# Kernel optimization log

Measured on AMD Instinct MI355X. Metric: run time of the kernel, lower is better.

## Reference

```python
import jax, jax.numpy as jnp
import numpy as np

B, S, D = 8, 8192, 64
N_HASHES = 8
BUCKET_SIZE = 64
N_BUCKETS = S // BUCKET_SIZE  # 128
SELF_ATTN_VALUE = -5e4  # torch reformer TOKEN_SELF_ATTN_VALUE


def setup_inputs() -> dict:
    key = jax.random.key(0)
    k1, k2, k3 = jax.random.split(key, 3)
    qk = jax.random.normal(k1, (B, S, D), dtype=jnp.float32)
    v = jax.random.normal(k2, (B, S, D), dtype=jnp.float32)
    # LSH random rotations: (dim, n_hashes, n_buckets // 2), shared across batch/heads
    rotations = jax.random.normal(k3, (D, N_HASHES, N_BUCKETS // 2), dtype=jnp.float32)
    return {"qk": qk, "v": v, "rotations": rotations, "query_len": S}


def _look_one_back(x):
    # concatenate each chunk with the preceding chunk (wrapping) along the kv axis
    x_extra = jnp.concatenate([x[:, -1:], x[:, :-1]], axis=1)
    return jnp.concatenate([x, x_extra], axis=2)


def _lsh_bucketed_dots(qk, v, rotations):
    batch, seqlen, dim = qk.shape
    n_buckets = seqlen // BUCKET_SIZE
    # --- hash vectors: rotate, concat with negation, argmax -> bucket ids ---
    rotated = jnp.einsum('btf,fhi->bhti', qk, rotations)           # (B, H, S, nb/2)
    rotated = jnp.concatenate([rotated, -rotated], axis=-1)        # (B, H, S, nb)
    buckets = jnp.argmax(rotated, axis=-1)                         # (B, H, S) int
    offsets = (jnp.arange(N_HASHES) * n_buckets)[None, :, None]    # disjoint per round
    buckets = (buckets + offsets).reshape(batch, -1)               # (B, H*S)

    # --- stable bucket sort via composite key (all keys unique) ---
    ticker = jnp.arange(N_HASHES * seqlen)[None, :]                # (1, H*S)
    buckets_and_t = seqlen * buckets + (ticker % seqlen)
    sticker = jnp.argsort(buckets_and_t, axis=-1)                  # sort permutation
    undo_sort = jnp.argsort(sticker, axis=-1)                      # inverse permutation
    st = sticker % seqlen                                          # original token ids

    # --- gather tokens into bucket order ---
    sqk = jnp.take_along_axis(qk, st[..., None], axis=1)           # (B, H*S, D)
    sv = jnp.take_along_axis(v, st[..., None], axis=1)

    n_chunks = N_HASHES * n_buckets
    bq_t = st.reshape(batch, n_chunks, BUCKET_SIZE)                # (B, C, bs)
    bqk = sqk.reshape(batch, n_chunks, BUCKET_SIZE, dim)
    bv = sv.reshape(batch, n_chunks, BUCKET_SIZE, dim)

    bq = bqk
    bk = bqk / (jnp.linalg.norm(bqk, axis=-1, keepdims=True) + 1e-6)  # unit-length keys

    bk = _look_one_back(bk)       # (B, C, 2*bs, D)
    bv = _look_one_back(bv)
    bkv_t = _look_one_back(bq_t)  # (B, C, 2*bs)

    dots = jnp.einsum('buie,buje->buij', bq, bk) * (dim ** -0.5)   # (B, C, bs, 2*bs)
    self_mask = bq_t[:, :, :, None] == bkv_t[:, :, None, :]
    dots = jnp.where(self_mask, SELF_ATTN_VALUE, dots)
    return dots, undo_sort, bv


def reference(qk, v, rotations, query_len):
    batch, seqlen, dim = qk.shape
    dots, undo_sort, bv = _lsh_bucketed_dots(qk, v, rotations)
    dots_logsumexp = jax.nn.logsumexp(dots, axis=-1, keepdims=True)
    p = jnp.exp(dots - dots_logsumexp)                             # per-bucket softmax
    bo = jnp.einsum('buij,buje->buie', p, bv)                      # (B, C, bs, D)
    so = bo.reshape(batch, -1, dim)                                # (B, H*S, D)
    slogits = dots_logsumexp.reshape(batch, -1)                    # (B, H*S)
    # undo the bucket sort
    o = jnp.take_along_axis(so, undo_sort[..., None], axis=1)
    logits = jnp.take_along_axis(slogits, undo_sort, axis=1)
    o = o.reshape(batch, N_HASHES, seqlen, dim)[:, :, :query_len]
    logits = logits.reshape(batch, N_HASHES, seqlen, 1)[:, :, :query_len]
    # combine across hash rounds, weighted by per-round logsumexp
    probs = jnp.exp(logits - jax.nn.logsumexp(logits, axis=1, keepdims=True))
    out = jnp.sum(o * probs, axis=1)                               # (B, query_len, D)
    return out
```

## Files before the change

kernel.cpp:

```cpp
#include <hip/hip_runtime.h>
#include <math.h>

#define B_  8
#define S_  8192
#define D_  64
#define H_  8
#define NB_ 128
#define NC_ 1024
#define REP_CAP 65536
#define T2_ 2e-3f

typedef _Float16 f16x8 __attribute__((ext_vector_type(8)));
typedef _Float16 f16x2 __attribute__((ext_vector_type(2)));
typedef float    f32x4 __attribute__((ext_vector_type(4)));
typedef unsigned int uint_;

#define MFMA16(A, Bv, C) __builtin_amdgcn_mfma_f32_16x16x32_f16(A, Bv, C, 0, 0, 0)

__global__ __launch_bounds__(256) void prep_rot_kernel(
    const float* __restrict__ rot, _Float16* __restrict__ rotHi,
    _Float16* __restrict__ rotLo, int* __restrict__ cnt)
{
  __shared__ float rs[64 * 64];
  const int tid = threadIdx.x, h = blockIdx.x;
  if (h == 0 && tid == 0) *cnt = 0;
#pragma unroll
  for (int it = 0; it < 16; ++it) {
    const int f = it * 4 + (tid >> 6), i = tid & 63;
    rs[f * 64 + i] = rot[f * 512 + h * 64 + i];
  }
  __syncthreads();
  const int i = tid & 63, grp = tid >> 6;
  _Float16 hi[16], lo[16];
#pragma unroll
  for (int ff = 0; ff < 16; ++ff) {
    const float x = rs[(grp * 16 + ff) * 64 + i];
    hi[ff] = (_Float16)x;
    lo[ff] = (_Float16)(x - (float)hi[ff]);
  }
  f16x8* dH = (f16x8*)(rotHi + h * 4096 + i * 64 + grp * 16);
  f16x8* dL = (f16x8*)(rotLo + h * 4096 + i * 64 + grp * 16);
  dH[0] = ((f16x8*)hi)[0]; dH[1] = ((f16x8*)hi)[1];
  dL[0] = ((f16x8*)lo)[0]; dL[1] = ((f16x8*)lo)[1];
}

__global__ __launch_bounds__(256) void prep_tok_kernel(
    const float* __restrict__ qk, const float* __restrict__ v,
    _Float16* __restrict__ q16, _Float16* __restrict__ kn16,
    _Float16* __restrict__ v16)
{
  const int gt = blockIdx.x * 64 + (threadIdx.x >> 2);
  const int qu = threadIdx.x & 3;
  const size_t off = (size_t)gt * 64 + qu * 16;
  float x[16];
#pragma unroll
  for (int k = 0; k < 4; ++k) ((float4*)x)[k] = ((const float4*)(qk + off))[k];
  float ss = 0.f;
#pragma unroll
  for (int k = 0; k < 16; ++k) ss = fmaf(x[k], x[k], ss);
  ss += __shfl_xor(ss, 1); ss += __shfl_xor(ss, 2);
  const float inv = 0.125f / (sqrtf(ss) + 1e-6f);
  f16x8 qh[2], kn[2];
#pragma unroll
  for (int j = 0; j < 16; ++j) {
    qh[j >> 3][j & 7] = (_Float16)x[j];
    kn[j >> 3][j & 7] = (_Float16)(x[j] * inv);
  }
  ((f16x8*)(q16  + off))[0] = qh[0]; ((f16x8*)(q16  + off))[1] = qh[1];
  ((f16x8*)(kn16 + off))[0] = kn[0]; ((f16x8*)(kn16 + off))[1] = kn[1];
  float y[16];
#pragma unroll
  for (int k = 0; k < 4; ++k) ((float4*)y)[k] = ((const float4*)(v + off))[k];
  f16x8 vv[2];
#pragma unroll
  for (int j = 0; j < 16; ++j) vv[j >> 3][j & 7] = (_Float16)y[j];
  ((f16x8*)(v16 + off))[0] = vv[0]; ((f16x8*)(v16 + off))[1] = vv[1];
}

__global__ __launch_bounds__(256) void hash_kernel(
    const float* __restrict__ qk,
    const _Float16* __restrict__ rotHi, const _Float16* __restrict__ rotLo,
    int* __restrict__ bucket, int* __restrict__ cnt, int2* __restrict__ list)
{
  __shared__ _Float16 rH[64 * 72];
  __shared__ _Float16 rL[64 * 72];
  const int tid  = threadIdx.x;
  const int tile = blockIdx.x & 127;
  const int b    = blockIdx.x >> 7;
  const int lane = tid & 63, w = tid >> 6;
  const int m16  = lane & 15, qd = lane >> 4;

  const int t = tile * 64 + w * 16 + m16;
  f16x8 BH0, BH1, BL0, BL1;
  {
    const float* src = qk + ((size_t)b * S_ + t) * 64 + 8 * qd;
    float x[16];
    ((float4*)x)[0] = ((const float4*)src)[0];
    ((float4*)x)[1] = ((const float4*)(src + 4))[0];
    ((float4*)x)[2] = ((const float4*)(src + 32))[0];
    ((float4*)x)[3] = ((const float4*)(src + 36))[0];
#pragma unroll
    for (int j = 0; j < 8; ++j) {
      const _Float16 h0 = (_Float16)x[j];
      BH0[j] = h0; BL0[j] = (_Float16)(x[j] - (float)h0);
      const _Float16 h1 = (_Float16)x[j + 8];
      BH1[j] = h1; BL1[j] = (_Float16)(x[j + 8] - (float)h1);
    }
  }
  const int srow = tid >> 2, scol = (tid & 3) * 16;
  const uint_ qd16 = (uint_)(qd << 4);

#pragma unroll 1
  for (int h = 0; h < 8; ++h) {
    __syncthreads();
    {
      const _Float16* sH = rotHi + h * 4096 + srow * 64 + scol;
      const _Float16* sL = rotLo + h * 4096 + srow * 64 + scol;
      *(f16x8*)(rH + srow * 72 + scol)     = ((const f16x8*)sH)[0];
      *(f16x8*)(rH + srow * 72 + scol + 8) = ((const f16x8*)sH)[1];
      *(f16x8*)(rL + srow * 72 + scol)     = ((const f16x8*)sL)[0];
      *(f16x8*)(rL + srow * 72 + scol + 8) = ((const f16x8*)sL)[1];
    }
    __syncthreads();

    f32x4 acc[4];
#pragma unroll
    for (int mt = 0; mt < 4; ++mt) acc[mt] = (f32x4){0.f, 0.f, 0.f, 0.f};
#pragma unroll
    for (int mt = 0; mt < 4; ++mt) {
      const _Float16* aH = rH + (16 * mt + m16) * 72 + 8 * qd;
      const _Float16* aL = rL + (16 * mt + m16) * 72 + 8 * qd;
      const f16x8 AH0 = *(const f16x8*)aH;
      const f16x8 AH1 = *(const f16x8*)(aH + 32);
      const f16x8 AL0 = *(const f16x8*)aL;
      const f16x8 AL1 = *(const f16x8*)(aL + 32);
      acc[mt] = MFMA16(AH0, BH0, acc[mt]);
      acc[mt] = MFMA16(AH1, BH1, acc[mt]);
      acc[mt] = MFMA16(AH0, BL0, acc[mt]);
      acc[mt] = MFMA16(AH1, BL1, acc[mt]);
      acc[mt] = MFMA16(AL0, BH0, acc[mt]);
      acc[mt] = MFMA16(AL1, BH1, acc[mt]);
    }

    float v1M = -1e30f, v2M = -1e30f, v1m = 1e30f, v2m = 1e30f;
#pragma unroll
    for (int mt = 0; mt < 4; ++mt)
#pragma unroll
      for (int rg = 0; rg < 4; ++rg) {
        uint_ u = __float_as_uint(acc[mt][rg]);
        u = (u & 0xFFFFFFC0u) | qd16 | (uint_)((mt << 2) | rg);
        const float xk = __uint_as_float(u);
        v2M = __builtin_amdgcn_fmed3f(v1M, v2M, xk);
        v1M = fmaxf(v1M, xk);
        v2m = __builtin_amdgcn_fmed3f(v1m, v2m, xk);
        v1m = fminf(v1m, xk);
      }
#pragma unroll
    for (int off = 16; off <= 32; off <<= 1) {
      const float o1M = __shfl_xor(v1M, off), o2M = __shfl_xor(v2M, off);
      v2M = __builtin_amdgcn_fmed3f(v1M, o1M, fmaxf(v2M, o2M));
      v1M = fmaxf(v1M, o1M);
      const float o1m = __shfl_xor(v1m, off), o2m = __shfl_xor(v2m, off);
      v2m = __builtin_amdgcn_fmed3f(v1m, o1m, fminf(v2m, o2m));
      v1m = fminf(v1m, o1m);
    }
    if (qd == 0) {
      const uint_ cM = __float_as_uint(v1M) & 63u;
      const uint_ cm = __float_as_uint(v1m) & 63u;
      const int ixM = 16 * (int)((cM >> 2) & 3u) + 4 * (int)(cM >> 4) + (int)(cM & 3u);
      const int ixm = 16 * (int)((cm >> 2) & 3u) + 4 * (int)(cm >> 4) + (int)(cm & 3u);
      const int bkt = (v1M >= -v1m) ? ixM : 64 + ixm;
      bucket[((size_t)(b * 8 + h)) * S_ + t] = bkt;
      const bool flag = ((v1M - v2M) < T2_) | ((v2m - v1m) < T2_) |
                        (fabsf(v1M + v1m) < T2_);
      if (flag) {
        const int s = atomicAdd(cnt, 1);
        if (s < REP_CAP) list[s] = make_int2(b * 8 + h, t);
      }
    }
  }
}

__global__ __launch_bounds__(256) void repair_kernel(
    const float* __restrict__ qk, const float* __restrict__ rot,
    const int* __restrict__ cnt, const int2* __restrict__ list,
    int* __restrict__ bucket)
{
  const int n = min(*cnt, REP_CAP);
  const int lane = threadIdx.x & 63;
  const int wid  = (blockIdx.x * 256 + threadIdx.x) >> 6;
  const int nw   = gridDim.x * 4;
  for (int idx = wid; idx < n; idx += nw) {
    const int bh = list[idx].x, t = list[idx].y;
    const int b = bh >> 3, hh = bh & 7;
    const float* qrow = qk + ((size_t)b * S_ + t) * D_;
    const float* rcol = rot + hh * 64 + lane;
    double acc = 0.0;
#pragma unroll 8
    for (int f = 0; f < 64; ++f)
      acc = fma((double)qrow[f], (double)rcol[(size_t)f * 512], acc);
    double vM = acc; int iM = lane;
    double vm = acc; int im = lane;
#pragma unroll
    for (int off = 32; off >= 1; off >>= 1) {
      const double voM = __shfl_xor(vM, off); const int ioM = __shfl_xor(iM, off);
      if (voM > vM || (voM == vM && ioM < iM)) { vM = voM; iM = ioM; }
      const double vom = __shfl_xor(vm, off); const int iom = __shfl_xor(im, off);
      if (vom < vm || (vom == vm && iom < im)) { vm = vom; im = iom; }
    }
    if (lane == 0) {
      const int bkt = (vM >= -vm) ? iM : 64 + im;
      bucket[(size_t)bh * S_ + t] = bkt;
    }
  }
}

__global__ __launch_bounds__(1024) void sort_kernel(
    const int* __restrict__ bucket, int* __restrict__ st)
{
  __shared__ uint_ hist[64 * 128];
  __shared__ unsigned short lb[S_];
  __shared__ int off[128];
  const int tid = threadIdx.x;
  const int bh  = blockIdx.x;
  const size_t base = (size_t)bh * S_;

#pragma unroll
  for (int k = 0; k < 8; ++k) hist[tid + k * 1024] = 0;
  __syncthreads();

#pragma unroll
  for (int k = 0; k < 8; ++k) {
    const int t = k * 1024 + tid;
    const int bk = bucket[base + t];
    lb[t] = (unsigned short)bk;
    const int g = t >> 6;
    atomicAdd(&hist[(g & 63) * 128 + bk], 1u << (16 * (g >> 6)));
  }
  __syncthreads();

  if (tid < 128) {
    uint_ s = 0;
#pragma unroll
    for (int g = 0; g < 64; ++g) {
      const uint_ wv = hist[g * 128 + tid];
      s += (wv & 0xFFFFu) + (wv >> 16);
    }
    off[tid] = (int)s;
  }
  __syncthreads();
  if (tid == 0) {
    int run = 0;
    for (int k = 0; k < 128; ++k) { const int c = off[k]; off[k] = run; run += c; }
  }
  __syncthreads();
  if (tid < 128) {
    uint_ run = (uint_)off[tid];
#pragma unroll
    for (int g = 0; g < 64; ++g) {
      const uint_ wv = hist[g * 128 + tid];
      hist[g * 128 + tid] = (wv & 0xFFFF0000u) | run;
      run += (wv & 0xFFFFu);
    }
#pragma unroll
    for (int g = 0; g < 64; ++g) {
      const uint_ wv = hist[g * 128 + tid];
      hist[g * 128 + tid] = (wv & 0xFFFFu) | (run << 16);
      run += (wv >> 16);
    }
  }
  __syncthreads();

  const int lane = tid & 63, wv_ = tid >> 6;
  const int b = bh >> 3, h = bh & 7;
  const size_t stb = (size_t)b * (H_ * S_) + (size_t)h * S_;
  const unsigned long long ltmask = (1ull << lane) - 1ull;
#pragma unroll
  for (int k = 0; k < 8; ++k) {
    const int g = wv_ * 8 + k;
    const int t = g * 64 + lane;
    const int bk = (int)lb[t];
    unsigned long long same = ~0ull;
#pragma unroll
    for (int bit = 0; bit < 7; ++bit) {
      const unsigned long long m = __ballot((bk >> bit) & 1);
      same &= ((bk >> bit) & 1) ? m : ~m;
    }
    const int rloc = __popcll(same & ltmask);
    const uint_ wd = hist[(g & 63) * 128 + bk];
    const int gbase = (int)((wd >> (16 * (g >> 6))) & 0xFFFFu);
    st[stb + gbase + rloc] = t;
  }
}

__global__ __launch_bounds__(256, 4) void attn_kernel(
    const _Float16* __restrict__ q16, const _Float16* __restrict__ kn16,
    const _Float16* __restrict__ v16, const int* __restrict__ st,
    _Float16* __restrict__ so, float* __restrict__ slog)
{
  __shared__ _Float16 sQ[64 * 72];
  __shared__ _Float16 sK[64 * 72];
  __shared__ _Float16 sP[64 * 136];
  __shared__ int sIds[128];

  const int tid = threadIdx.x;
  const int c   = blockIdx.x & (NC_ - 1);
  const int b   = blockIdx.x >> 10;
  const int cm1 = (c + NC_ - 1) & (NC_ - 1);
  const size_t bst = (size_t)b * (H_ * S_);
  const size_t row0 = bst + (size_t)c * 64;
  const size_t row1 = bst + (size_t)cm1 * 64;

  const int lane = tid & 63;
  const int w    = tid >> 6;
  const int m16  = lane & 15;
  const int qd   = lane >> 4;

  if (tid < 128) sIds[tid] = (tid < 64) ? st[row0 + tid] : st[row1 + tid - 64];

  const int r = tid >> 2, qu = tid & 3;
  {
    const int tok = st[row0 + r];
    const size_t go = ((size_t)b * S_ + tok) * 64 + qu * 16;
    const f16x8* sq = (const f16x8*)(q16 + go);
    *(f16x8*)(sQ + r * 72 + qu * 16)     = sq[0];
    *(f16x8*)(sQ + r * 72 + qu * 16 + 8) = sq[1];
    const f16x8* sk = (const f16x8*)(kn16 + go);
    *(f16x8*)(sK + r * 72 + qu * 16)     = sk[0];
    *(f16x8*)(sK + r * 72 + qu * 16 + 8) = sk[1];
  }
  __syncthreads();

  f32x4 acc[8];
#pragma unroll
  for (int jt = 0; jt < 8; ++jt) acc[jt] = (f32x4){0.f, 0.f, 0.f, 0.f};

  const _Float16* qrow = sQ + (16 * w + m16) * 72;
  const f16x8 a0 = *(const f16x8*)(qrow + 8 * qd);
  const f16x8 a1 = *(const f16x8*)(qrow + 32 + 8 * qd);

#pragma unroll
  for (int jt = 0; jt < 4; ++jt) {
    const _Float16* krow = sK + (16 * jt + m16) * 72;
    const f16x8 b0 = *(const f16x8*)(krow + 8 * qd);
    const f16x8 b1 = *(const f16x8*)(krow + 32 + 8 * qd);
    acc[jt] = MFMA16(a0, b0, acc[jt]);
    acc[jt] = MFMA16(a1, b1, acc[jt]);
  }
  __syncthreads();

  {
    const int tok = st[row1 + r];
    const f16x8* sk = (const f16x8*)(kn16 + ((size_t)b * S_ + tok) * 64 + qu * 16);
    *(f16x8*)(sK + r * 72 + qu * 16)     = sk[0];
    *(f16x8*)(sK + r * 72 + qu * 16 + 8) = sk[1];
  }
  __syncthreads();

#pragma unroll
  for (int jt = 4; jt < 8; ++jt) {
    const _Float16* krow = sK + (16 * (jt - 4) + m16) * 72;
    const f16x8 b0 = *(const f16x8*)(krow + 8 * qd);
    const f16x8 b1 = *(const f16x8*)(krow + 32 + 8 * qd);
    acc[jt] = MFMA16(a0, b0, acc[jt]);
    acc[jt] = MFMA16(a1, b1, acc[jt]);
  }

  const int jp = tid >> 2;
  const int tok0 = sIds[2 * jp], tok1 = sIds[2 * jp + 1];
  f16x8 va[2], vb[2];
  {
    const f16x8* s0 = (const f16x8*)(v16 + ((size_t)b * S_ + tok0) * 64 + qu * 16);
    const f16x8* s1 = (const f16x8*)(v16 + ((size_t)b * S_ + tok1) * 64 + qu * 16);
    va[0] = s0[0]; va[1] = s0[1];
    vb[0] = s1[0]; vb[1] = s1[1];
  }

  int rid[4];
#pragma unroll
  for (int rg = 0; rg < 4; ++rg) rid[rg] = sIds[16 * w + 4 * qd + rg];
  float rmax[4] = {-1e30f, -1e30f, -1e30f, -1e30f};
#pragma unroll
  for (int jt = 0; jt < 8; ++jt) {
    const int cid = sIds[16 * jt + m16];
#pragma unroll
    for (int rg = 0; rg < 4; ++rg) {
      float x = acc[jt][rg];
      if (rid[rg] == cid) x = -5e4f;
      acc[jt][rg] = x;
      rmax[rg] = fmaxf(rmax[rg], x);
    }
  }
#pragma unroll
  for (int rg = 0; rg < 4; ++rg) {
    rmax[rg] = fmaxf(rmax[rg], __shfl_xor(rmax[rg], 1));
    rmax[rg] = fmaxf(rmax[rg], __shfl_xor(rmax[rg], 2));
    rmax[rg] = fmaxf(rmax[rg], __shfl_xor(rmax[rg], 4));
    rmax[rg] = fmaxf(rmax[rg], __shfl_xor(rmax[rg], 8));
  }
  float rsum[4] = {0.f, 0.f, 0.f, 0.f};
#pragma unroll
  for (int jt = 0; jt < 8; ++jt)
#pragma unroll
    for (int rg = 0; rg < 4; ++rg) {
      const float e = __expf(acc[jt][rg] - rmax[rg]);
      acc[jt][rg] = e;
      rsum[rg] += e;
    }
#pragma unroll
  for (int rg = 0; rg < 4; ++rg) {
    rsum[rg] += __shfl_xor(rsum[rg], 1);
    rsum[rg] += __shfl_xor(rsum[rg], 2);
    rsum[rg] += __shfl_xor(rsum[rg], 4);
    rsum[rg] += __shfl_xor(rsum[rg], 8);
  }
  float rinv[4];
#pragma unroll
  for (int rg = 0; rg < 4; ++rg) rinv[rg] = 1.f / rsum[rg];

  const int hh = c >> 7;
  const size_t hb = ((size_t)(b * 8 + hh)) * S_;
  if (m16 == 0) {
#pragma unroll
    for (int rg = 0; rg < 4; ++rg)
      slog[hb + rid[rg]] = rmax[rg] + __logf(rsum[rg]);
  }

#pragma unroll
  for (int jt = 0; jt < 8; ++jt)
#pragma unroll
    for (int rg = 0; rg < 4; ++rg)
      sP[(16 * w + 4 * qd + rg) * 136 + 16 * jt + m16] = (_Float16)acc[jt][rg];

  __syncthreads();

  {
    const int j = 2 * jp;
    _Float16* dst = (j < 64) ? (sK + j) : (sQ + (j - 64));
#pragma unroll
    for (int jj = 0; jj < 16; ++jj) {
      const int d = qu * 16 + jj;
      f16x2 pk; pk[0] = va[jj >> 3][jj & 7]; pk[1] = vb[jj >> 3][jj & 7];
      *(f16x2*)(dst + d * 72) = pk;
    }
  }
  __syncthreads();

  f32x4 oacc[4];
#pragma unroll
  for (int dt = 0; dt < 4; ++dt) oacc[dt] = (f32x4){0.f, 0.f, 0.f, 0.f};
  const _Float16* prow = sP + (16 * w + m16) * 136;
#pragma unroll
  for (int s = 0; s < 4; ++s) {
    const f16x8 ap = *(const f16x8*)(prow + 32 * s + 8 * qd);
    const _Float16* vbase = (s < 2) ? sK : sQ;
    const int col0 = 32 * (s & 1) + 8 * qd;
#pragma unroll
    for (int dt = 0; dt < 4; ++dt) {
      const f16x8 bv = *(const f16x8*)(vbase + (16 * dt + m16) * 72 + col0);
      oacc[dt] = MFMA16(ap, bv, oacc[dt]);
    }
  }

#pragma unroll
  for (int dt = 0; dt < 4; ++dt)
#pragma unroll
    for (int rg = 0; rg < 4; ++rg)
      so[(hb + rid[rg]) * 64 + 16 * dt + m16] = (_Float16)(oacc[dt][rg] * rinv[rg]);
}

__global__ __launch_bounds__(256) void combine_kernel(
    const _Float16* __restrict__ so, const float* __restrict__ slog,
    float* __restrict__ out)
{
  const int gt = blockIdx.x * 4 + (threadIdx.x >> 6);
  const int d  = threadIdx.x & 63;
  const int b  = gt >> 13;
  const int t  = gt & (S_ - 1);

  float l[8];
#pragma unroll
  for (int h = 0; h < 8; ++h)
    l[h] = slog[((size_t)(b * 8 + h)) * S_ + t];
  float m = l[0];
#pragma unroll
  for (int h = 1; h < 8; ++h) m = fmaxf(m, l[h]);
  float wv[8], W = 0.f;
#pragma unroll
  for (int h = 0; h < 8; ++h) { wv[h] = expf(l[h] - m); W += wv[h]; }
  const float iW = 1.f / W;
  float acc = 0.f;
#pragma unroll
  for (int h = 0; h < 8; ++h)
    acc = fmaf(wv[h], (float)so[(((size_t)(b * 8 + h)) * S_ + t) * 64 + d], acc);
  out[(size_t)gt * 64 + d] = acc * iW;
}

extern "C" void kernel_launch(void* const* d_in, const int* in_sizes, int n_in,
                              void* d_out, int out_size, void* d_ws, size_t ws_size,
                              hipStream_t stream)
{
  const float* qk  = (const float*)d_in[0];
  const float* v   = (const float*)d_in[1];
  const float* rot = (const float*)d_in[2];
  float* out = (float*)d_out;

  char* ws = (char*)d_ws;
  const size_t MB = 1ull << 20, KB = 1024;
  int*      bucket = (int*)      (ws + 0 * MB);
  int*      st     = (int*)      (ws + 2 * MB);
  float*    slog   = (float*)    (ws + 4 * MB);
  _Float16* q16    = (_Float16*) (ws + 8 * MB);
  _Float16* kn16   = (_Float16*) (ws + 16 * MB);
  _Float16* v16    = (_Float16*) (ws + 24 * MB);
  _Float16* rotHi  = (_Float16*) (ws + 32 * MB);
  _Float16* rotLo  = (_Float16*) (ws + 32 * MB + 64 * KB);
  int*      cnt    = (int*)      (ws + 32 * MB + 128 * KB);
  int2*     list   = (int2*)     (ws + 32 * MB + 192 * KB);
  _Float16* so     = (_Float16*) (ws + 33 * MB);
  if (ws_size < 98 * MB) return;

  hipLaunchKernelGGL(prep_rot_kernel, dim3(8),           dim3(256),  0, stream, rot, rotHi, rotLo, cnt);
  hipLaunchKernelGGL(prep_tok_kernel, dim3(1024),        dim3(256),  0, stream, qk, v, q16, kn16, v16);
  hipLaunchKernelGGL(hash_kernel,     dim3(8 * 128),     dim3(256),  0, stream, qk, rotHi, rotLo, bucket, cnt, list);
  hipLaunchKernelGGL(repair_kernel,   dim3(128),         dim3(256),  0, stream, qk, rot, cnt, list, bucket);
  hipLaunchKernelGGL(sort_kernel,     dim3(64),          dim3(1024), 0, stream, bucket, st);
  hipLaunchKernelGGL(attn_kernel,     dim3(B_ * NC_),    dim3(256),  0, stream, q16, kn16, v16, st, so, slog);
  hipLaunchKernelGGL(combine_kernel,  dim3(B_ * S_ / 4), dim3(256),  0, stream, so, slog, out);
}
```

Measured before the change: 209.2 us.

## Fuse token fp16 prep into hash kernel, read rotations directly, stage attn output

Merges prep_tok_kernel into hash_kernel so qk is read once and q16/kn16/v16 are written from the same loads, removing a launch and a full pass over qk. The rotation tiles are no longer staged through LDS with barriers; each wave loads rotation fragments straight from global/L2. The attention output is now staged through shared memory so the global scatter into so writes contiguous 32-byte rows per thread. Direct global rotation loads add L2 traffic per block, and the fused kernel carries more registers.

```diff
diff --git a/kernel.cpp b/kernel.cpp
--- a/kernel.cpp
+++ b/kernel.cpp
@@ -44,46 +44,13 @@
   dL[0] = ((f16x8*)lo)[0]; dL[1] = ((f16x8*)lo)[1];
 }
 
-__global__ __launch_bounds__(256) void prep_tok_kernel(
+__global__ __launch_bounds__(256) void hash_kernel(
     const float* __restrict__ qk, const float* __restrict__ v,
+    const _Float16* __restrict__ rotHi, const _Float16* __restrict__ rotLo,
     _Float16* __restrict__ q16, _Float16* __restrict__ kn16,
-    _Float16* __restrict__ v16)
-{
-  const int gt = blockIdx.x * 64 + (threadIdx.x >> 2);
-  const int qu = threadIdx.x & 3;
-  const size_t off = (size_t)gt * 64 + qu * 16;
-  float x[16];
-#pragma unroll
-  for (int k = 0; k < 4; ++k) ((float4*)x)[k] = ((const float4*)(qk + off))[k];
-  float ss = 0.f;
-#pragma unroll
-  for (int k = 0; k < 16; ++k) ss = fmaf(x[k], x[k], ss);
-  ss += __shfl_xor(ss, 1); ss += __shfl_xor(ss, 2);
-  const float inv = 0.125f / (sqrtf(ss) + 1e-6f);
-  f16x8 qh[2], kn[2];
-#pragma unroll
-  for (int j = 0; j < 16; ++j) {
-    qh[j >> 3][j & 7] = (_Float16)x[j];
-    kn[j >> 3][j & 7] = (_Float16)(x[j] * inv);
-  }
-  ((f16x8*)(q16  + off))[0] = qh[0]; ((f16x8*)(q16  + off))[1] = qh[1];
-  ((f16x8*)(kn16 + off))[0] = kn[0]; ((f16x8*)(kn16 + off))[1] = kn[1];
-  float y[16];
-#pragma unroll
-  for (int k = 0; k < 4; ++k) ((float4*)y)[k] = ((const float4*)(v + off))[k];
-  f16x8 vv[2];
-#pragma unroll
-  for (int j = 0; j < 16; ++j) vv[j >> 3][j & 7] = (_Float16)y[j];
-  ((f16x8*)(v16 + off))[0] = vv[0]; ((f16x8*)(v16 + off))[1] = vv[1];
-}
-
-__global__ __launch_bounds__(256) void hash_kernel(
-    const float* __restrict__ qk,
-    const _Float16* __restrict__ rotHi, const _Float16* __restrict__ rotLo,
+    _Float16* __restrict__ v16,
     int* __restrict__ bucket, int* __restrict__ cnt, int2* __restrict__ list)
 {
-  __shared__ _Float16 rH[64 * 72];
-  __shared__ _Float16 rL[64 * 72];
   const int tid  = threadIdx.x;
   const int tile = blockIdx.x & 127;
   const int b    = blockIdx.x >> 7;
@@ -91,49 +58,65 @@
   const int m16  = lane & 15, qd = lane >> 4;
 
   const int t = tile * 64 + w * 16 + m16;
+  const size_t rowo = ((size_t)b * S_ + t) * 64;
+
   f16x8 BH0, BH1, BL0, BL1;
   {
-    const float* src = qk + ((size_t)b * S_ + t) * 64 + 8 * qd;
+    const float* src = qk + rowo + 8 * qd;
     float x[16];
     ((float4*)x)[0] = ((const float4*)src)[0];
     ((float4*)x)[1] = ((const float4*)(src + 4))[0];
     ((float4*)x)[2] = ((const float4*)(src + 32))[0];
     ((float4*)x)[3] = ((const float4*)(src + 36))[0];
+    float ss = 0.f;
+#pragma unroll
+    for (int j = 0; j < 16; ++j) ss = fmaf(x[j], x[j], ss);
+    ss += __shfl_xor(ss, 16); ss += __shfl_xor(ss, 32);
+    const float inv = 0.125f / (sqrtf(ss) + 1e-6f);
+    f16x8 KN0, KN1;
 #pragma unroll
     for (int j = 0; j < 8; ++j) {
       const _Float16 h0 = (_Float16)x[j];
       BH0[j] = h0; BL0[j] = (_Float16)(x[j] - (float)h0);
       const _Float16 h1 = (_Float16)x[j + 8];
       BH1[j] = h1; BL1[j] = (_Float16)(x[j + 8] - (float)h1);
-    }
-  }
-  const int srow = tid >> 2, scol = (tid & 3) * 16;
+      KN0[j] = (_Float16)(x[j] * inv);
+      KN1[j] = (_Float16)(x[j + 8] * inv);
+    }
+    *(f16x8*)(q16 + rowo + 8 * qd)       = BH0;
+    *(f16x8*)(q16 + rowo + 32 + 8 * qd)  = BH1;
+    *(f16x8*)(kn16 + rowo + 8 * qd)      = KN0;
+    *(f16x8*)(kn16 + rowo + 32 + 8 * qd) = KN1;
+  }
+  {
+    const float* src = v + rowo + 8 * qd;
+    float y[16];
+    ((float4*)y)[0] = ((const float4*)src)[0];
+    ((float4*)y)[1] = ((const float4*)(src + 4))[0];
+    ((float4*)y)[2] = ((const float4*)(src + 32))[0];
+    ((float4*)y)[3] = ((const float4*)(src + 36))[0];
+    f16x8 V0, V1;
+#pragma unroll
+    for (int j = 0; j < 8; ++j) { V0[j] = (_Float16)y[j]; V1[j] = (_Float16)y[j + 8]; }
+    *(f16x8*)(v16 + rowo + 8 * qd)      = V0;
+    *(f16x8*)(v16 + rowo + 32 + 8 * qd) = V1;
+  }
+
   const uint_ qd16 = (uint_)(qd << 4);
-
 #pragma unroll 1
   for (int h = 0; h < 8; ++h) {
-    __syncthreads();
-    {
-      const _Float16* sH = rotHi + h * 4096 + srow * 64 + scol;
-      const _Float16* sL = rotLo + h * 4096 + srow * 64 + scol;
-      *(f16x8*)(rH + srow * 72 + scol)     = ((const f16x8*)sH)[0];
-      *(f16x8*)(rH + srow * 72 + scol + 8) = ((const f16x8*)sH)[1];
-      *(f16x8*)(rL + srow * 72 + scol)     = ((const f16x8*)sL)[0];
-      *(f16x8*)(rL + srow * 72 + scol + 8) = ((const f16x8*)sL)[1];
-    }
-    __syncthreads();
-
+    const _Float16* rbH = rotHi + h * 4096;
+    const _Float16* rbL = rotLo + h * 4096;
     f32x4 acc[4];
 #pragma unroll
     for (int mt = 0; mt < 4; ++mt) acc[mt] = (f32x4){0.f, 0.f, 0.f, 0.f};
 #pragma unroll
     for (int mt = 0; mt < 4; ++mt) {
-      const _Float16* aH = rH + (16 * mt + m16) * 72 + 8 * qd;
-      const _Float16* aL = rL + (16 * mt + m16) * 72 + 8 * qd;
-      const f16x8 AH0 = *(const f16x8*)aH;
-      const f16x8 AH1 = *(const f16x8*)(aH + 32);
-      const f16x8 AL0 = *(const f16x8*)aL;
-      const f16x8 AL1 = *(const f16x8*)(aL + 32);
+      const int row = (16 * mt + m16) * 64 + 8 * qd;
+      const f16x8 AH0 = *(const f16x8*)(rbH + row);
+      const f16x8 AH1 = *(const f16x8*)(rbH + row + 32);
+      const f16x8 AL0 = *(const f16x8*)(rbL + row);
+      const f16x8 AL1 = *(const f16x8*)(rbL + row + 32);
       acc[mt] = MFMA16(AH0, BH0, acc[mt]);
       acc[mt] = MFMA16(AH1, BH1, acc[mt]);
       acc[mt] = MFMA16(AH0, BL0, acc[mt]);
@@ -466,7 +449,16 @@
   for (int dt = 0; dt < 4; ++dt)
 #pragma unroll
     for (int rg = 0; rg < 4; ++rg)
-      so[(hb + rid[rg]) * 64 + 16 * dt + m16] = (_Float16)(oacc[dt][rg] * rinv[rg]);
+      sP[(16 * w + 4 * qd + rg) * 136 + 16 * dt + m16] =
+          (_Float16)(oacc[dt][rg] * rinv[rg]);
+  {
+    const int r2 = tid >> 2, c4 = tid & 3;
+    const f16x8 o0 = *(const f16x8*)(sP + r2 * 136 + c4 * 16);
+    const f16x8 o1 = *(const f16x8*)(sP + r2 * 136 + c4 * 16 + 8);
+    _Float16* dst = so + (hb + sIds[r2]) * 64 + c4 * 16;
+    ((f16x8*)dst)[0] = o0;
+    ((f16x8*)dst)[1] = o1;
+  }
 }
 
 __global__ __launch_bounds__(256) void combine_kernel(
@@ -521,8 +513,8 @@
   if (ws_size < 98 * MB) return;
 
   hipLaunchKernelGGL(prep_rot_kernel, dim3(8),           dim3(256),  0, stream, rot, rotHi, rotLo, cnt);
-  hipLaunchKernelGGL(prep_tok_kernel, dim3(1024),        dim3(256),  0, stream, qk, v, q16, kn16, v16);
-  hipLaunchKernelGGL(hash_kernel,     dim3(8 * 128),     dim3(256),  0, stream, qk, rotHi, rotLo, bucket, cnt, list);
+  hipLaunchKernelGGL(hash_kernel,     dim3(8 * 128),     dim3(256),  0, stream, qk, v, rotHi, rotLo,
+                     q16, kn16, v16, bucket, cnt, list);
   hipLaunchKernelGGL(repair_kernel,   dim3(128),         dim3(256),  0, stream, qk, rot, cnt, list, bucket);
   hipLaunchKernelGGL(sort_kernel,     dim3(64),          dim3(1024), 0, stream, bucket, st);
   hipLaunchKernelGGL(attn_kernel,     dim3(B_ * NC_),    dim3(256),  0, stream, q16, kn16, v16, st, so, slog);
```

After: 241.2 us. +15.3%, slower.
